# Kernel tuning notes

Hardware: AMD Instinct MI355X
Metric: run time of the kernel (lower is better)

## Reference

```python
import jax, jax.numpy as jnp
import numpy as np

N, E = 50000, 800000
D_IN, HID, H, C, E_DIM = 128, 128, 4, 32, 32  # C = HID // H


def setup_inputs() -> dict:
    key = jax.random.key(0)
    ks = jax.random.split(key, 16)
    def lin(k, fan_in, fan_out):
        return jax.random.normal(k, (fan_in, fan_out), jnp.float32) / np.sqrt(fan_in)
    return {
        "x": jax.random.normal(ks[0], (N, D_IN), jnp.float32),
        "edge_index": jax.random.randint(ks[1], (2, E), 0, N, jnp.int32),
        "edge_attr": jax.random.normal(ks[2], (E, E_DIM), jnp.float32),
        # TransformerConv params (bias=True on q/k/v and skip; lin_edge has no bias in PyG)
        "Wq": lin(ks[3], D_IN, HID), "bq": jnp.zeros((HID,), jnp.float32),
        "Wk": lin(ks[4], D_IN, HID), "bk": jnp.zeros((HID,), jnp.float32),
        "Wv": lin(ks[5], D_IN, HID), "bv": jnp.zeros((HID,), jnp.float32),
        "We": lin(ks[6], E_DIM, HID),
        "Wskip": lin(ks[7], D_IN, HID), "bskip": jnp.zeros((HID,), jnp.float32),
        # MLP([HID, HID, HID]) -> two Linear layers, GELU(tanh) after each (plain_last=False)
        "W1": lin(ks[8], HID, HID), "b1": jnp.zeros((HID,), jnp.float32),
        "W2": lin(ks[9], HID, HID), "b2": jnp.zeros((HID,), jnp.float32),
    }


def reference(x, edge_index, edge_attr, Wq, bq, Wk, bk, Wv, bv, We, Wskip, bskip, W1, b1, W2, b2):
    src, dst = edge_index[0], edge_index[1]  # messages flow src(j) -> dst(i)
    n = x.shape[0]
    q = (x @ Wq + bq).reshape(n, H, C)
    k = (x @ Wk + bk).reshape(n, H, C)
    v = (x @ Wv + bv).reshape(n, H, C)
    e = (edge_attr @ We).reshape(-1, H, C)          # [E,H,C]
    kj = k[src] + e                                  # gather + edge lift
    vj = v[src] + e
    alpha = jnp.einsum("ehc,ehc->eh", q[dst], kj) / np.sqrt(C)  # [E,H]
    # segment softmax over destination neighborhoods (PyG softmax semantics)
    amax = jax.ops.segment_max(alpha, dst, num_segments=n)      # [N,H]
    amax = jnp.where(jnp.isfinite(amax), amax, 0.0)
    ex = jnp.exp(alpha - amax[dst])
    denom = jax.ops.segment_sum(ex, dst, num_segments=n)
    alpha = ex / (denom[dst] + 1e-16)
    # (attention dropout p=0.3 is inactive in eval mode)
    agg = jax.ops.segment_sum(vj * alpha[:, :, None], dst, num_segments=n)  # [N,H,C]
    out = agg.reshape(n, HID) + (x @ Wskip + bskip)  # concat heads + root skip
    # residual MLP: gelu(tanh) after every layer since plain_last=False, norm=None
    h = jax.nn.gelu(out @ W1 + b1, approximate=True)
    h = jax.nn.gelu(h @ W2 + b2, approximate=True)
    return out + h
```

## Files before the change

kernel.cpp:

```cpp
#include <hip/hip_runtime.h>
#include <math.h>


#define D 128
#define EDIM 32

using bf16x8 = __attribute__((ext_vector_type(8))) short;
using f32x4  = __attribute__((ext_vector_type(4))) float;
using ushort8 = __attribute__((ext_vector_type(8))) unsigned short;

__device__ inline unsigned short f2bf(float f) {
    unsigned int u = __float_as_uint(f);
    u += 0x7FFFu + ((u >> 16) & 1u);
    return (unsigned short)(u >> 16);
}
__device__ inline float bf2f(unsigned short h) {
    return __uint_as_float(((unsigned int)h) << 16);
}
__device__ inline float gelu_fast(float x) {
    float x3 = x * x * x;
    float u = 0.7978845608028654f * (x + 0.044715f * x3);
    float t = 1.f - 2.f / (__expf(2.f * u) + 1.f);
    return 0.5f * x * (1.f + t);
}
__device__ inline float quad_add(float x) {
    int a = __builtin_amdgcn_update_dpp(0, __float_as_int(x), 0xB1, 0xF, 0xF, true);
    x += __int_as_float(a);
    a = __builtin_amdgcn_update_dpp(0, __float_as_int(x), 0x4E, 0xF, 0xF, true);
    x += __int_as_float(a);
    return x;
}

__device__ inline bf16x8 ldsB(const unsigned short* sw, int col, int kk0) {
    return *(const bf16x8*)(sw + col * 128 + (kk0 ^ ((col & 7) << 3)));
}

__global__ __launch_bounds__(256) void prep_kernel(
    const float* __restrict__ Wq, const float* __restrict__ Wk,
    const float* __restrict__ Wv, const float* __restrict__ Wsk,
    const float* __restrict__ W1, const float* __restrict__ W2,
    const float* __restrict__ We, const float* __restrict__ bq,
    unsigned short* __restrict__ Wt, float* __restrict__ bqE,
    const int* __restrict__ EI, int* __restrict__ deg, int E, int HB,
    const float* __restrict__ x, unsigned short* __restrict__ XB, long xtot)
{
    if ((int)blockIdx.x >= 513 + HB) {
        long i8 = ((long)(blockIdx.x - 513 - HB) * 256 + threadIdx.x) * 8;
        if (i8 + 8 <= xtot) {
            float4 a = *(const float4*)(x + i8);
            float4 b = *(const float4*)(x + i8 + 4);
            ushort8 u;
            u[0] = f2bf(a.x); u[1] = f2bf(a.y); u[2] = f2bf(a.z); u[3] = f2bf(a.w);
            u[4] = f2bf(b.x); u[5] = f2bf(b.y); u[6] = f2bf(b.z); u[7] = f2bf(b.w);
            *(ushort8*)(XB + i8) = u;
        }
        return;
    }
    if (blockIdx.x >= 513) {
        int e = (blockIdx.x - 513) * 256 + threadIdx.x;
        if (e < E) atomicAdd(&deg[EI[E + e]], 1);
        return;
    }
    int t = blockIdx.x * 256 + threadIdx.x;
    int m = t >> 14;
    int r = t & 16383;
    if (m >= 8) {
        if (r < 128) {
            const int hb = r & 96, k = r & 31;
            const float* wek = We + (size_t)k * D + hb;
            float s = 0.f;
#pragma unroll 8
            for (int c = 0; c < 32; ++c) s = fmaf(bq[hb + c], wek[c], s);
            bqE[r] = s;
        }
        return;
    }
    int col = r & 127, kk = r >> 7;
    float v;
    if (m < 6) {
        const float* W = (m == 0) ? Wq : (m == 1) ? Wk : (m == 2) ? Wv
                       : (m == 3) ? Wsk : (m == 4) ? W1 : W2;
        v = W[(size_t)kk * D + col];
    } else if (m == 6) {
        const int hb = col & 96;
        const float* wqr = Wq + (size_t)kk * D + hb;
        const float* wer = We + (size_t)(col & 31) * D + hb;
        float s = 0.f;
#pragma unroll 8
        for (int c = 0; c < 32; ++c) s = fmaf(wqr[c], wer[c], s);
        v = s;
    } else {
        v = ((kk >> 5) == (col >> 5)) ? We[(size_t)(kk & 31) * D + col] : 0.f;
    }
    Wt[(size_t)m * 16384 + (size_t)col * 128 + (kk ^ ((col & 7) << 3))] = f2bf(v);
}

__global__ __launch_bounds__(1024) void scanA(
    const int* __restrict__ deg, int* __restrict__ rowptr,
    int* __restrict__ psums, int N)
{
    __shared__ int tmp[1024];
    const int t = threadIdx.x;
    const int i = blockIdx.x * 1024 + t;
    int v = (i < N) ? deg[i] : 0;
    tmp[t] = v;
    __syncthreads();
    for (int off = 1; off < 1024; off <<= 1) {
        int add = (t >= off) ? tmp[t - off] : 0;
        __syncthreads();
        tmp[t] += add;
        __syncthreads();
    }
    if (i < N) rowptr[i + 1] = tmp[t];
    if (t == 1023) psums[blockIdx.x] = tmp[1023];
}

__global__ __launch_bounds__(1024) void scanB(int* __restrict__ psums, int nb)
{
    __shared__ int tmp[1024];
    const int t = threadIdx.x;
    int v = (t < nb) ? psums[t] : 0;
    tmp[t] = v;
    __syncthreads();
    for (int off = 1; off < 1024; off <<= 1) {
        int add = (t >= off) ? tmp[t - off] : 0;
        __syncthreads();
        tmp[t] += add;
        __syncthreads();
    }
    if (t < nb) psums[t] = tmp[t] - v;
}

__global__ __launch_bounds__(256) void scanC(
    int* __restrict__ rowptr, int* __restrict__ cursor,
    const int* __restrict__ psums, int N)
{
    int i = blockIdx.x * 256 + threadIdx.x;
    if (i == 0) { rowptr[0] = 0; cursor[0] = 0; }
    if (i < N) {
        int val = rowptr[i + 1] + psums[i >> 10];
        rowptr[i + 1] = val;
        if (i + 1 < N) cursor[i + 1] = val;
    }
}

__global__ __launch_bounds__(256) void mega_gemm_scatter(
    const unsigned short* __restrict__ XB, const unsigned short* __restrict__ Wt,
    const float* __restrict__ bq, const float* __restrict__ bk,
    const float* __restrict__ bv, const float* __restrict__ bs,
    const float* __restrict__ bqE,
    unsigned short* __restrict__ QA, unsigned short* __restrict__ KV,
    float* __restrict__ S, int N, int NB2,
    const int* __restrict__ EI, int* __restrict__ cursor,
    int2* __restrict__ SE, int E)
{
    __shared__ unsigned short sw[16384];
    const int t = threadIdx.x;

    if ((int)blockIdx.x >= 5 * NB2) {
        int e = (blockIdx.x - 5 * NB2) * 256 + t;
        if (e < E) {
            int dst = EI[E + e];
            int pos = atomicAdd(&cursor[dst], 1);
            SE[pos] = make_int2(EI[e], e);
        }
        return;
    }

    const int bid = blockIdx.x;
    const int m = bid / NB2;
    const int bx = bid - m * NB2;
    const int widx = (m < 4) ? m : 6;
    const int lane = t & 63;
    const int w = t >> 6;
    const int row0 = bx * 128 + w * 32;
    const int lrow = lane & 15;
    const int kb = (lane >> 4) * 8;
    const int rq = (lane >> 4) * 4;

    const unsigned short* gsrc = Wt + (size_t)widx * 16384;
    ushort8 stg[8];
#pragma unroll
    for (int it = 0; it < 8; ++it)
        stg[it] = *(const ushort8*)(gsrc + (t + it * 256) * 8);

    bf16x8 af0[4], af1[4];
    {
        int a0 = row0 + lrow;      if (a0 > N - 1) a0 = N - 1;
        int a1 = row0 + 16 + lrow; if (a1 > N - 1) a1 = N - 1;
        const unsigned short* x0 = XB + (size_t)a0 * D + kb;
        const unsigned short* x1 = XB + (size_t)a1 * D + kb;
#pragma unroll
        for (int kf = 0; kf < 4; ++kf) {
            af0[kf] = *(const bf16x8*)(x0 + kf * 32);
            af1[kf] = *(const bf16x8*)(x1 + kf * 32);
        }
    }

#pragma unroll
    for (int it = 0; it < 8; ++it)
        *(ushort8*)(&sw[(t + it * 256) * 8]) = stg[it];
    __syncthreads();

    const float* bias = (m == 0) ? bq : (m == 1) ? bk : (m == 2) ? bv
                      : (m == 3) ? bs : bqE;
    f32x4 acc0[8], acc1[8];
#pragma unroll
    for (int nf = 0; nf < 8; ++nf) {
        acc0[nf] = (f32x4){0.f, 0.f, 0.f, 0.f};
        acc1[nf] = (f32x4){0.f, 0.f, 0.f, 0.f};
    }
#pragma unroll
    for (int nf = 0; nf < 8; ++nf) {
        const int col = nf * 16 + lrow;
#pragma unroll
        for (int kf = 0; kf < 4; ++kf) {
            bf16x8 bfr = ldsB(sw, col, kf * 32 + kb);
            acc0[nf] = __builtin_amdgcn_mfma_f32_16x16x32_bf16(af0[kf], bfr, acc0[nf], 0, 0, 0);
            acc1[nf] = __builtin_amdgcn_mfma_f32_16x16x32_bf16(af1[kf], bfr, acc1[nf], 0, 0, 0);
        }
    }
#pragma unroll
    for (int rb = 0; rb < 2; ++rb) {
#pragma unroll
        for (int nf = 0; nf < 8; ++nf) {
            const int col = nf * 16 + lrow;
            const float bb = bias[col];
#pragma unroll
            for (int i = 0; i < 4; ++i) {
                int r = row0 + rb * 16 + rq + i;
                if (r < N) {
                    float v = ((rb == 0) ? acc0[nf][i] : acc1[nf][i]) + bb;
                    if (m == 0)      QA[(size_t)r * 256 + col]       = f2bf(v);
                    else if (m == 1) KV[(size_t)r * 256 + col]       = f2bf(v);
                    else if (m == 2) KV[(size_t)r * 256 + 128 + col] = f2bf(v);
                    else if (m == 3) S[(size_t)r * D + col]          = v;
                    else             QA[(size_t)r * 256 + 128 + col] = f2bf(v);
                }
            }
        }
    }
}

__global__ __launch_bounds__(256) void gather_pass(
    const int* __restrict__ rowptr, const int2* __restrict__ SE,
    const float* __restrict__ EA,
    const unsigned short* __restrict__ QA, const unsigned short* __restrict__ KV,
    float* __restrict__ SB, unsigned short* __restrict__ SAS, int N)
{
    const int lane = threadIdx.x & 63;
    const int wid = threadIdx.x >> 6;
    const int n = blockIdx.x * 4 + wid;
    if (n >= N) return;
    const int g = lane & 15;
    const int grp = lane >> 4;
    const int eoff = (g & 3) * 8;

    float q8[8], qe8[8];
    {
        const unsigned short* qa = QA + (size_t)n * 256 + g * 8;
        bf16x8 qb  = *(const bf16x8*)(qa);
        bf16x8 qeb = *(const bf16x8*)(qa + 128);
#pragma unroll
        for (int j = 0; j < 8; ++j) {
            q8[j]  = bf2f((unsigned short)qb[j]);
            qe8[j] = bf2f((unsigned short)qeb[j]);
        }
    }

    float acc[8], sa[8], den = 0.f;
#pragma unroll
    for (int j = 0; j < 8; ++j) { acc[j] = 0.f; sa[j] = 0.f; }

    const int i0 = rowptr[n], i1 = rowptr[n + 1];

    int iA = i0 + grp, iB = iA + 4;
    int2 seA = (iA < i1) ? SE[iA] : make_int2(-1, 0);
    int2 seB = (iB < i1) ? SE[iB] : make_int2(-1, 0);

    for (int b = i0; b < i1; b += 8) {
        const int iA2 = iA + 8, iB2 = iB + 8;
        const int2 seA2 = (iA2 < i1) ? SE[iA2] : make_int2(-1, 0);
        const int2 seB2 = (iB2 < i1) ? SE[iB2] : make_int2(-1, 0);

        bf16x8 kA = {0,0,0,0,0,0,0,0}, vA = kA;
        bf16x8 kB = kA, vB = kA;
        float4 eA0 = {0,0,0,0}, eA1 = eA0, eB0 = eA0, eB1 = eA0;
        if (seA.x >= 0) {
            const unsigned short* kv = KV + (size_t)seA.x * 256 + g * 8;
            kA = *(const bf16x8*)(kv);
            vA = *(const bf16x8*)(kv + 128);
            const float* ear = EA + (size_t)seA.y * EDIM + eoff;
            eA0 = *(const float4*)(ear);
            eA1 = *(const float4*)(ear + 4);
        }
        if (seB.x >= 0) {
            const unsigned short* kv = KV + (size_t)seB.x * 256 + g * 8;
            kB = *(const bf16x8*)(kv);
            vB = *(const bf16x8*)(kv + 128);
            const float* ear = EA + (size_t)seB.y * EDIM + eoff;
            eB0 = *(const float4*)(ear);
            eB1 = *(const float4*)(ear + 4);
        }

        {
            float ef[8] = {eA0.x, eA0.y, eA0.z, eA0.w, eA1.x, eA1.y, eA1.z, eA1.w};
            float p = 0.f;
#pragma unroll
            for (int j = 0; j < 8; ++j)
                p = fmaf(q8[j], bf2f((unsigned short)kA[j]),
                         fmaf(ef[j], qe8[j], p));
            p = quad_add(p);
            const float ex = (seA.x >= 0) ? __expf(p * 0.17677669529663689f) : 0.f;
            den += ex;
#pragma unroll
            for (int j = 0; j < 8; ++j) {
                acc[j] = fmaf(ex, bf2f((unsigned short)vA[j]), acc[j]);
                sa[j]  = fmaf(ex, ef[j], sa[j]);
            }
        }
        {
            float ef[8] = {eB0.x, eB0.y, eB0.z, eB0.w, eB1.x, eB1.y, eB1.z, eB1.w};
            float p = 0.f;
#pragma unroll
            for (int j = 0; j < 8; ++j)
                p = fmaf(q8[j], bf2f((unsigned short)kB[j]),
                         fmaf(ef[j], qe8[j], p));
            p = quad_add(p);
            const float ex = (seB.x >= 0) ? __expf(p * 0.17677669529663689f) : 0.f;
            den += ex;
#pragma unroll
            for (int j = 0; j < 8; ++j) {
                acc[j] = fmaf(ex, bf2f((unsigned short)vB[j]), acc[j]);
                sa[j]  = fmaf(ex, ef[j], sa[j]);
            }
        }
        iA = iA2; iB = iB2; seA = seA2; seB = seB2;
    }

#pragma unroll
    for (int off = 16; off <= 32; off <<= 1) {
        den += __shfl_xor(den, off, 64);
#pragma unroll
        for (int j = 0; j < 8; ++j) {
            acc[j] += __shfl_xor(acc[j], off, 64);
            sa[j]  += __shfl_xor(sa[j],  off, 64);
        }
    }

    if (grp == 0) {
        const float rden = 1.f / (den + 1e-16f);
        float* so = SB + (size_t)n * D + g * 8;
        unsigned short* po = SAS + (size_t)n * D + g * 8;
#pragma unroll
        for (int j = 0; j < 8; ++j) {
            so[j] = fmaf(acc[j], rden, so[j]);
            po[j] = f2bf(sa[j] * rden);
        }
    }
}

__global__ __launch_bounds__(256) void fused_mlp(
    const float* __restrict__ SB, const unsigned short* __restrict__ SAS,
    const unsigned short* __restrict__ WtC, const unsigned short* __restrict__ Wt1,
    const unsigned short* __restrict__ Wt2,
    const float* __restrict__ b1, const float* __restrict__ b2,
    float* __restrict__ FINAL, int N)
{
    __shared__ unsigned short sw[16384];
    __shared__ unsigned short bounce[64 * 136];
    const int t = threadIdx.x;
    const int lane = t & 63;
    const int w = t >> 6;
    const int row0 = blockIdx.x * 64 + w * 16;
    const int lrow = lane & 15;
    const int kb = (lane >> 4) * 8;
    const int rq = (lane >> 4) * 4;

    ushort8 stg[8];
#pragma unroll
    for (int it = 0; it < 8; ++it)
        stg[it] = *(const ushort8*)(WtC + (t + it * 256) * 8);

    bf16x8 af[4];
    {
        int ar = row0 + lrow; if (ar > N - 1) ar = N - 1;
        const unsigned short* xr = SAS + (size_t)ar * D + kb;
#pragma unroll
        for (int kf = 0; kf < 4; ++kf) af[kf] = *(const bf16x8*)(xr + kf * 32);
    }
    f32x4 out[8];
#pragma unroll
    for (int nf = 0; nf < 8; ++nf) {
        const int col = nf * 16 + lrow;
#pragma unroll
        for (int i = 0; i < 4; ++i) {
            int r = row0 + rq + i;
            out[nf][i] = (r < N) ? SB[(size_t)r * D + col] : 0.f;
        }
    }
#pragma unroll
    for (int it = 0; it < 8; ++it)
        *(ushort8*)(&sw[(t + it * 256) * 8]) = stg[it];
    __syncthreads();

#pragma unroll
    for (int nf = 0; nf < 8; ++nf) {
        const int col = nf * 16 + lrow;
#pragma unroll
        for (int kf = 0; kf < 4; ++kf)
            out[nf] = __builtin_amdgcn_mfma_f32_16x16x32_bf16(
                af[kf], ldsB(sw, col, kf * 32 + kb), out[nf], 0, 0, 0);
    }
    __syncthreads();

#pragma unroll
    for (int it = 0; it < 8; ++it)
        stg[it] = *(const ushort8*)(Wt1 + (t + it * 256) * 8);
#pragma unroll
    for (int nf = 0; nf < 8; ++nf) {
        const int col = nf * 16 + lrow;
#pragma unroll
        for (int i = 0; i < 4; ++i)
            bounce[(w * 16 + rq + i) * 136 + col] = f2bf(out[nf][i]);
    }
#pragma unroll
    for (int it = 0; it < 8; ++it)
        *(ushort8*)(&sw[(t + it * 256) * 8]) = stg[it];
    __syncthreads();

    bf16x8 af2[4];
#pragma unroll
    for (int kf = 0; kf < 4; ++kf)
        af2[kf] = *(const bf16x8*)(&bounce[(w * 16 + lrow) * 136 + kb + kf * 32]);
    f32x4 acc2[8];
#pragma unroll
    for (int nf = 0; nf < 8; ++nf) acc2[nf] = (f32x4){0.f, 0.f, 0.f, 0.f};
#pragma unroll
    for (int nf = 0; nf < 8; ++nf) {
        const int col = nf * 16 + lrow;
#pragma unroll
        for (int kf = 0; kf < 4; ++kf)
            acc2[nf] = __builtin_amdgcn_mfma_f32_16x16x32_bf16(
                af2[kf], ldsB(sw, col, kf * 32 + kb), acc2[nf], 0, 0, 0);
    }
    __syncthreads();

#pragma unroll
    for (int it = 0; it < 8; ++it)
        stg[it] = *(const ushort8*)(Wt2 + (t + it * 256) * 8);
#pragma unroll
    for (int nf = 0; nf < 8; ++nf) {
        const int col = nf * 16 + lrow;
        const float bb = b1[col];
#pragma unroll
        for (int i = 0; i < 4; ++i)
            bounce[(w * 16 + rq + i) * 136 + col] = f2bf(gelu_fast(acc2[nf][i] + bb));
    }
#pragma unroll
    for (int it = 0; it < 8; ++it)
        *(ushort8*)(&sw[(t + it * 256) * 8]) = stg[it];
    __syncthreads();

    bf16x8 af3[4];
#pragma unroll
    for (int kf = 0; kf < 4; ++kf)
        af3[kf] = *(const bf16x8*)(&bounce[(w * 16 + lrow) * 136 + kb + kf * 32]);
    f32x4 acc3[8];
#pragma unroll
    for (int nf = 0; nf < 8; ++nf) acc3[nf] = (f32x4){0.f, 0.f, 0.f, 0.f};
#pragma unroll
    for (int nf = 0; nf < 8; ++nf) {
        const int col = nf * 16 + lrow;
#pragma unroll
        for (int kf = 0; kf < 4; ++kf)
            acc3[nf] = __builtin_amdgcn_mfma_f32_16x16x32_bf16(
                af3[kf], ldsB(sw, col, kf * 32 + kb), acc3[nf], 0, 0, 0);
    }
#pragma unroll
    for (int nf = 0; nf < 8; ++nf) {
        const int col = nf * 16 + lrow;
        const float bb = b2[col];
#pragma unroll
        for (int i = 0; i < 4; ++i) {
            int r = row0 + rq + i;
            if (r < N)
                FINAL[(size_t)r * D + col] = out[nf][i] + gelu_fast(acc3[nf][i] + bb);
        }
    }
}

extern "C" void kernel_launch(void* const* d_in, const int* in_sizes, int n_in,
                              void* d_out, int out_size, void* d_ws, size_t ws_size,
                              hipStream_t stream)
{
    const float* x   = (const float*)d_in[0];
    const int*   EI  = (const int*)  d_in[1];
    const float* EA  = (const float*)d_in[2];
    const float* Wq  = (const float*)d_in[3];
    const float* bq  = (const float*)d_in[4];
    const float* Wk  = (const float*)d_in[5];
    const float* bk  = (const float*)d_in[6];
    const float* Wv  = (const float*)d_in[7];
    const float* bv  = (const float*)d_in[8];
    const float* We  = (const float*)d_in[9];
    const float* Wsk = (const float*)d_in[10];
    const float* bsk = (const float*)d_in[11];
    const float* W1  = (const float*)d_in[12];
    const float* b1  = (const float*)d_in[13];
    const float* W2  = (const float*)d_in[14];
    const float* b2  = (const float*)d_in[15];

    const int N = in_sizes[0] / D;
    const int E = in_sizes[1] / 2;

    char* p = (char*)d_ws;
    auto alloc = [&](size_t bytes) -> void* {
        void* r = (void*)p;
        p += (bytes + 255) & ~(size_t)255;
        return r;
    };
    float*          Sb     = (float*)         alloc((size_t)N * D * 4);
    unsigned short* QAb    = (unsigned short*)alloc((size_t)N * 256 * 2);
    unsigned short* KVb    = (unsigned short*)alloc((size_t)N * 256 * 2);
    unsigned short* SASb   = (unsigned short*)alloc((size_t)N * D * 2);
    unsigned short* XBb    = (unsigned short*)alloc((size_t)N * D * 2);
    int2*           SEb    = (int2*)          alloc((size_t)E * 8);
    unsigned short* Wt     = (unsigned short*)alloc((size_t)8 * 16384 * 2);
    float*          bqEb   = (float*)         alloc((size_t)128 * 4);
    int*            deg    = (int*)           alloc((size_t)N * 4);
    int*            rowptr = (int*)           alloc((size_t)(N + 1) * 4);
    int*            cursor = (int*)           alloc((size_t)(N + 1) * 4);
    int*            psums  = (int*)           alloc((size_t)1024 * 4);

    hipMemsetAsync(deg, 0, (size_t)N * sizeof(int), stream);

    const long xtot = (long)N * D;
    const int NB  = (N + 63) / 64;
    const int NB2 = (N + 127) / 128;
    const int EB  = (E + 255) / 256;
    const int XB_ = (int)((xtot + 2047) / 2048);
    const int SB_ = (N + 1023) / 1024;

    prep_kernel<<<513 + EB + XB_, 256, 0, stream>>>(
        Wq, Wk, Wv, Wsk, W1, W2, We, bq, Wt, bqEb, EI, deg, E, EB, x, XBb, xtot);

    scanA<<<SB_, 1024, 0, stream>>>(deg, rowptr, psums, N);
    scanB<<<1, 1024, 0, stream>>>(psums, SB_);
    scanC<<<(N + 255) / 256, 256, 0, stream>>>(rowptr, cursor, psums, N);

    mega_gemm_scatter<<<5 * NB2 + EB, 256, 0, stream>>>(
        XBb, Wt, bq, bk, bv, bsk, bqEb, QAb, KVb, Sb, N, NB2,
        EI, cursor, SEb, E);

    gather_pass<<<(N + 3) / 4, 256, 0, stream>>>(
        rowptr, SEb, EA, QAb, KVb, Sb, SASb, N);

    fused_mlp<<<NB, 256, 0, stream>>>(Sb, SASb,
                                      Wt + (size_t)7 * 16384,
                                      Wt + (size_t)4 * 16384,
                                      Wt + (size_t)5 * 16384,
                                      b1, b2, (float*)d_out, N);
}
```

Baseline: 279.7 us.

## Split edge scatter from GEMM kernel and stage bf16 outputs through LDS

The fused GEMM+scatter launch is split into a separate scatter kernel and a pure 5-way GEMM kernel. For the bf16 outputs (Q, K, V, Q·We), results are first written to shared memory and then stored to global memory as 16-byte vectors per row, replacing scattered 2-byte stores. The fp32 skip output keeps its direct store path. This aims to raise store coalescing at the cost of an extra kernel launch and an LDS round trip with a barrier.

```diff
diff --git a/kernel.cpp b/kernel.cpp
--- a/kernel.cpp
+++ b/kernel.cpp
@@ -144,29 +144,28 @@
     }
 }
 
-__global__ __launch_bounds__(256) void mega_gemm_scatter(
+__global__ __launch_bounds__(256) void scatter_kernel(
+    const int* __restrict__ EI, int* __restrict__ cursor,
+    int2* __restrict__ SE, int E)
+{
+    int e = blockIdx.x * 256 + threadIdx.x;
+    if (e < E) {
+        int dst = EI[E + e];
+        int pos = atomicAdd(&cursor[dst], 1);
+        SE[pos] = make_int2(EI[e], e);
+    }
+}
+
+__global__ __launch_bounds__(256) void gemm5(
     const unsigned short* __restrict__ XB, const unsigned short* __restrict__ Wt,
     const float* __restrict__ bq, const float* __restrict__ bk,
     const float* __restrict__ bv, const float* __restrict__ bs,
     const float* __restrict__ bqE,
     unsigned short* __restrict__ QA, unsigned short* __restrict__ KV,
-    float* __restrict__ S, int N, int NB2,
-    const int* __restrict__ EI, int* __restrict__ cursor,
-    int2* __restrict__ SE, int E)
+    float* __restrict__ S, int N, int NB2)
 {
     __shared__ unsigned short sw[16384];
     const int t = threadIdx.x;
-
-    if ((int)blockIdx.x >= 5 * NB2) {
-        int e = (blockIdx.x - 5 * NB2) * 256 + t;
-        if (e < E) {
-            int dst = EI[E + e];
-            int pos = atomicAdd(&cursor[dst], 1);
-            SE[pos] = make_int2(EI[e], e);
-        }
-        return;
-    }
-
     const int bid = blockIdx.x;
     const int m = bid / NB2;
     const int bx = bid - m * NB2;
@@ -220,6 +219,26 @@
             acc1[nf] = __builtin_amdgcn_mfma_f32_16x16x32_bf16(af1[kf], bfr, acc1[nf], 0, 0, 0);
         }
     }
+
+    if (m == 3) {
+#pragma unroll
+        for (int rb = 0; rb < 2; ++rb) {
+#pragma unroll
+            for (int nf = 0; nf < 8; ++nf) {
+                const int col = nf * 16 + lrow;
+                const float bb = bias[col];
+#pragma unroll
+                for (int i = 0; i < 4; ++i) {
+                    int r = row0 + rb * 16 + rq + i;
+                    if (r < N)
+                        S[(size_t)r * D + col] = ((rb == 0) ? acc0[nf][i] : acc1[nf][i]) + bb;
+                }
+            }
+        }
+        return;
+    }
+
+    __syncthreads();
 #pragma unroll
     for (int rb = 0; rb < 2; ++rb) {
 #pragma unroll
@@ -227,18 +246,21 @@
             const int col = nf * 16 + lrow;
             const float bb = bias[col];
 #pragma unroll
-            for (int i = 0; i < 4; ++i) {
-                int r = row0 + rb * 16 + rq + i;
-                if (r < N) {
-                    float v = ((rb == 0) ? acc0[nf][i] : acc1[nf][i]) + bb;
-                    if (m == 0)      QA[(size_t)r * 256 + col]       = f2bf(v);
-                    else if (m == 1) KV[(size_t)r * 256 + col]       = f2bf(v);
-                    else if (m == 2) KV[(size_t)r * 256 + 128 + col] = f2bf(v);
-                    else if (m == 3) S[(size_t)r * D + col]          = v;
-                    else             QA[(size_t)r * 256 + 128 + col] = f2bf(v);
-                }
-            }
-        }
+            for (int i = 0; i < 4; ++i)
+                sw[(w * 32 + rb * 16 + rq + i) * 128 + col] =
+                    f2bf(((rb == 0) ? acc0[nf][i] : acc1[nf][i]) + bb);
+        }
+    }
+    unsigned short* gout = (m == 0) ? QA : (m == 1) ? KV
+                         : (m == 2) ? KV + 128 : QA + 128;
+#pragma unroll
+    for (int it = 0; it < 8; ++it) {
+        const int gidx = it * 64 + lane;
+        const int row_l = gidx >> 4;
+        const int chk = gidx & 15;
+        const int r = row0 + row_l;
+        ushort8 vv = *(const ushort8*)(&sw[(w * 32 + row_l) * 128 + chk * 8]);
+        if (r < N) *(ushort8*)(gout + (size_t)r * 256 + chk * 8) = vv;
     }
 }
 
@@ -549,9 +571,10 @@
     scanB<<<1, 1024, 0, stream>>>(psums, SB_);
     scanC<<<(N + 255) / 256, 256, 0, stream>>>(rowptr, cursor, psums, N);
 
-    mega_gemm_scatter<<<5 * NB2 + EB, 256, 0, stream>>>(
-        XBb, Wt, bq, bk, bv, bsk, bqEb, QAb, KVb, Sb, N, NB2,
-        EI, cursor, SEb, E);
+    scatter_kernel<<<EB, 256, 0, stream>>>(EI, cursor, SEb, E);
+
+    gemm5<<<5 * NB2, 256, 0, stream>>>(
+        XBb, Wt, bq, bk, bv, bsk, bqEb, QAb, KVb, Sb, N, NB2);
 
     gather_pass<<<(N + 3) / 4, 256, 0, stream>>>(
         rowptr, SEb, EA, QAb, KVb, Sb, SASb, N);
```

Result: faster. 265.7 us (-5.0%).
